# Optimization experiments

Measured on AMD Instinct MI355X. Metric: run time of the kernel, lower is better.

The kernel has to match this reference:

```python
import jax, jax.numpy as jnp
import numpy as np

B, S, H = 4, 2048, 2048          # batch, seq_len, hidden_size
NH, NKV, D = 8, 1, 256           # query heads, kv heads (MQA), head_dim
ROPE_THETA = 10000.0
SCALE = D ** -0.5


def setup_inputs() -> dict:
    key = jax.random.key(0)
    k1, k2, k3 = jax.random.split(key, 3)
    hidden_states = jax.random.normal(k1, (B, S, H), dtype=jnp.float32)
    w_qkv = jax.random.normal(k2, (H, (NH + 2 * NKV) * D), dtype=jnp.float32) * 0.02
    w_o = jax.random.normal(k3, (NH * D, H), dtype=jnp.float32) * 0.02
    positions = jnp.arange(S, dtype=jnp.int32)
    return {"hidden_states": hidden_states, "positions": positions,
            "w_qkv": w_qkv, "w_o": w_o}


def _apply_rope(x, positions):
    # x: [B, S, n_heads, D], neox style: rotate halves
    d2 = D // 2
    inv_freq = 1.0 / (ROPE_THETA ** (jnp.arange(0, d2, dtype=jnp.float32) * 2.0 / D))
    ang = positions.astype(jnp.float32)[:, None] * inv_freq[None, :]      # [S, d2]
    cos = jnp.cos(ang)[None, :, None, :]                                  # [1,S,1,d2]
    sin = jnp.sin(ang)[None, :, None, :]
    x1, x2 = x[..., :d2], x[..., d2:]
    return jnp.concatenate([x1 * cos - x2 * sin, x2 * cos + x1 * sin], axis=-1)


def reference(hidden_states, positions, w_qkv, w_o):
    # fused QKV projection
    qkv = jnp.einsum('bsh,hd->bsd', hidden_states, w_qkv)                 # [B,S,(NH+2NKV)*D]
    q_size, kv_size = NH * D, NKV * D
    q = qkv[..., :q_size].reshape(B, S, NH, D)
    k = qkv[..., q_size:q_size + kv_size].reshape(B, S, NKV, D)
    v = qkv[..., q_size + kv_size:].reshape(B, S, NKV, D)

    q = _apply_rope(q, positions)
    k = _apply_rope(k, positions)

    # expand KV heads for MQA/GQA
    rep = NH // NKV
    k = jnp.repeat(k, rep, axis=2)                                        # [B,S,NH,D]
    v = jnp.repeat(v, rep, axis=2)

    scores = jnp.einsum('bqhd,bkhd->bhqk', q, k) * SCALE                  # [B,NH,S,S]
    causal = jnp.tril(jnp.ones((S, S), dtype=bool))
    scores = jnp.where(causal[None, None], scores, jnp.finfo(scores.dtype).min)
    probs = jax.nn.softmax(scores, axis=-1)
    attn = jnp.einsum('bhqk,bkhd->bqhd', probs, v).reshape(B, S, NH * D)

    return jnp.einsum('bsd,dh->bsh', attn, w_o)                           # [B,S,H]
```

## Files before the change

kernel.cpp:

```cpp
#include <hip/hip_runtime.h>
#include <math.h>

constexpr int BATCH = 4;
constexpr int SEQ   = 2048;
constexpr int HID   = 2048;
constexpr int NHEAD = 8;
constexpr int HD    = 256;
constexpr int QKVN  = (NHEAD + 2) * HD;
constexpr float SCL = 0.0625f;

typedef __bf16 bf16_t;
typedef __bf16 bf16x8 __attribute__((ext_vector_type(8)));
typedef float  f32x4  __attribute__((ext_vector_type(4)));

__device__ __forceinline__ f32x4 zero4() {
  f32x4 z; z[0] = 0.f; z[1] = 0.f; z[2] = 0.f; z[3] = 0.f; return z;
}

__device__ __forceinline__ f32x4 mfma16(bf16x8 a, bf16x8 b, f32x4 c) {
  return __builtin_amdgcn_mfma_f32_16x16x32_bf16(a, b, c, 0, 0, 0);
}

__device__ __forceinline__ void gl2lds16(const void* g, void* lds) {
  typedef __attribute__((address_space(1))) void* gp_t;
  typedef __attribute__((address_space(3))) void* lp_t;
  __builtin_amdgcn_global_load_lds((gp_t)(size_t)g,
                                   (lp_t)(unsigned int)(size_t)lds, 16, 0, 0);
}

__device__ __forceinline__ float rmax16(float v) {
#pragma unroll
  for (int o = 1; o < 16; o <<= 1) v = fmaxf(v, __shfl_xor(v, o));
  return v;
}
__device__ __forceinline__ float rsum16(float v) {
#pragma unroll
  for (int o = 1; o < 16; o <<= 1) v += __shfl_xor(v, o);
  return v;
}

__global__ __launch_bounds__(256)
void cvt_bf16_kernel(const float* __restrict__ in, bf16_t* __restrict__ out) {
  const int i = blockIdx.x * 256 + threadIdx.x;
  const float4 a = ((const float4*)in)[i * 2];
  const float4 b = ((const float4*)in)[i * 2 + 1];
  bf16x8 o;
  o[0] = (bf16_t)a.x; o[1] = (bf16_t)a.y; o[2] = (bf16_t)a.z; o[3] = (bf16_t)a.w;
  o[4] = (bf16_t)b.x; o[5] = (bf16_t)b.y; o[6] = (bf16_t)b.z; o[7] = (bf16_t)b.w;
  ((bf16x8*)out)[i] = o;
}

__global__ __launch_bounds__(256)
void transw_kernel(const float* __restrict__ w, bf16_t* __restrict__ wT, int K, int N) {
  __shared__ __align__(16) bf16_t tile[64][72];
  const int n0 = blockIdx.x * 64, k0 = blockIdx.y * 64;
  const int t = threadIdx.x, rr = t >> 3, c8 = (t & 7) * 8;
#pragma unroll
  for (int it = 0; it < 2; ++it) {
    const int r = rr + it * 32;
    const float4* p = (const float4*)(w + (size_t)(k0 + r) * N + n0 + c8);
    const float4 a = p[0], b = p[1];
    bf16x8 o;
    o[0] = (bf16_t)a.x; o[1] = (bf16_t)a.y; o[2] = (bf16_t)a.z; o[3] = (bf16_t)a.w;
    o[4] = (bf16_t)b.x; o[5] = (bf16_t)b.y; o[6] = (bf16_t)b.z; o[7] = (bf16_t)b.w;
    *(bf16x8*)&tile[r][c8] = o;
  }
  __syncthreads();
#pragma unroll
  for (int it = 0; it < 2; ++it) {
    const int rn = rr + it * 32;
    bf16x8 o;
#pragma unroll
    for (int j = 0; j < 8; ++j) o[j] = tile[c8 + j][rn];
    *(bf16x8*)&wT[(size_t)(n0 + rn) * K + k0 + c8] = o;
  }
}

template <typename TC>
__global__ __launch_bounds__(256)
void gemm_bt_kernel(const bf16_t* __restrict__ A, const bf16_t* __restrict__ BT,
                    TC* __restrict__ C, int M, int N, int K) {
  __shared__ __align__(16) bf16_t As[128 * 32];
  __shared__ __align__(16) bf16_t Bs[128 * 32];
  const int tid = threadIdx.x;
  const int lane = tid & 63, w = tid >> 6;
  const int quad = lane >> 4, l15 = lane & 15;
  const int bm = blockIdx.y * 128, bn = blockIdx.x * 128;
  const int wm = (w & 1) * 64, wn = (w >> 1) * 64;
  const int r0 = tid >> 2, c0 = tid & 3;

  f32x4 acc[4][4];
#pragma unroll
  for (int mt = 0; mt < 4; ++mt)
#pragma unroll
    for (int nt = 0; nt < 4; ++nt) acc[mt][nt] = zero4();

  for (int k0 = 0; k0 < K; k0 += 32) {
#pragma unroll
    for (int i = 0; i < 2; ++i) {
      const int r = r0 + i * 64;
      const int cg = (c0 ^ (r & 3)) << 3;
      gl2lds16(A + (size_t)(bm + r) * K + k0 + cg, &As[(i * 256 + w * 64) * 8]);
      gl2lds16(BT + (size_t)(bn + r) * K + k0 + cg, &Bs[(i * 256 + w * 64) * 8]);
    }
    __syncthreads();
    bf16x8 af[4], bf[4];
#pragma unroll
    for (int mt = 0; mt < 4; ++mt) {
      const int row = wm + mt * 16 + l15;
      af[mt] = *(const bf16x8*)&As[row * 32 + ((quad ^ (row & 3)) << 3)];
    }
#pragma unroll
    for (int nt = 0; nt < 4; ++nt) {
      const int row = wn + nt * 16 + l15;
      bf[nt] = *(const bf16x8*)&Bs[row * 32 + ((quad ^ (row & 3)) << 3)];
    }
#pragma unroll
    for (int mt = 0; mt < 4; ++mt)
#pragma unroll
      for (int nt = 0; nt < 4; ++nt)
        acc[mt][nt] = mfma16(af[mt], bf[nt], acc[mt][nt]);
    __syncthreads();
  }

#pragma unroll
  for (int mt = 0; mt < 4; ++mt)
#pragma unroll
    for (int nt = 0; nt < 4; ++nt)
#pragma unroll
      for (int r = 0; r < 4; ++r) {
        const int row = bm + wm + mt * 16 + quad * 4 + r;
        const int col = bn + wn + nt * 16 + l15;
        C[(size_t)row * N + col] = (TC)acc[mt][nt][r];
      }
}

__global__ __launch_bounds__(128)
void rope_kernel(const int* __restrict__ pos, bf16_t* __restrict__ qkv) {
  const int bs = blockIdx.x, h = blockIdx.y, i = threadIdx.x;
  const int s = bs & (SEQ - 1);
  const float inv_freq = powf(10000.0f, -(float)i / 128.0f);
  const float ang = (float)pos[s] * inv_freq;
  float sn, cs;
  sincosf(ang, &sn, &cs);
  const size_t base = (size_t)bs * QKVN + (size_t)h * HD;
  const float x1 = (float)qkv[base + i];
  const float x2 = (float)qkv[base + 128 + i];
  qkv[base + i]       = (bf16_t)(x1 * cs - x2 * sn);
  qkv[base + 128 + i] = (bf16_t)(x2 * cs + x1 * sn);
}

__global__ __launch_bounds__(256)
void vtrans_kernel(const bf16_t* __restrict__ qkv, bf16_t* __restrict__ Vt) {
  __shared__ __align__(16) bf16_t tile[64][72];
  const int s0 = blockIdx.x * 64, d0 = blockIdx.y * 64, b = blockIdx.z;
  const int t = threadIdx.x, rr = t >> 3, c8 = (t & 7) * 8;
#pragma unroll
  for (int it = 0; it < 2; ++it) {
    const int r = rr + it * 32;
    *(bf16x8*)&tile[r][c8] =
        *(const bf16x8*)&qkv[(size_t)(b * SEQ + s0 + r) * QKVN + 2304 + d0 + c8];
  }
  __syncthreads();
#pragma unroll
  for (int it = 0; it < 2; ++it) {
    const int dd = rr + it * 32;
    bf16x8 o;
#pragma unroll
    for (int j = 0; j < 8; ++j) o[j] = tile[c8 + j][dd];
    *(bf16x8*)&Vt[(size_t)(b * HD + d0 + dd) * SEQ + s0 + c8] = o;
  }
}

__global__ __launch_bounds__(512)
void attn_kernel(const bf16_t* __restrict__ qkv, const bf16_t* __restrict__ Vt,
                 bf16_t* __restrict__ O) {
  __shared__ __align__(16) bf16_t Ks[64 * 256];
  __shared__ __align__(16) bf16_t Vts[256 * 64];
  __shared__ __align__(16) bf16_t Pl[8][16][72];

  const int tid = threadIdx.x, w = tid >> 6, lane = tid & 63;
  const int quad = lane >> 4, l15 = lane & 15;
  const int b = blockIdx.x >> 6;
  const int qtR = blockIdx.x & 63;
  const int h = w;

  const int krow_base = w * 2 + (lane >> 5);
  const int kcol = lane & 31;
  const int vrow_base = w * 8 + (lane >> 3);
  const int vcol = lane & 7;

  for (int phase = 0; phase < 2; ++phase) {
    const int qt = phase ? (127 - qtR) : qtR;
    const int q0 = qt * 16;

    bf16x8 qf[8];
    const bf16_t* qp =
        qkv + (size_t)(b * SEQ + q0 + l15) * QKVN + (size_t)h * HD + quad * 8;
#pragma unroll
    for (int ks = 0; ks < 8; ++ks) qf[ks] = *(const bf16x8*)(qp + ks * 32);

    float mrun[4], lrun[4];
    f32x4 of[16];
#pragma unroll
    for (int r = 0; r < 4; ++r) { mrun[r] = -3e38f; lrun[r] = 0.f; }
#pragma unroll
    for (int dt = 0; dt < 16; ++dt) of[dt] = zero4();

    const int ntiles = q0 / 64 + 1;

    for (int kt = 0; kt < ntiles; ++kt) {
      const bf16_t* kbase = qkv + (size_t)(b * SEQ + kt * 64) * QKVN + 2048;
#pragma unroll
      for (int i = 0; i < 4; ++i) {
        const int r = i * 16 + krow_base;
        gl2lds16(kbase + (size_t)r * QKVN + ((kcol ^ (r & 31)) << 3),
                 &Ks[(i * 512 + w * 64) * 8]);
      }
      const bf16_t* vbase = Vt + (size_t)b * HD * SEQ + kt * 64;
#pragma unroll
      for (int i = 0; i < 4; ++i) {
        const int r = i * 64 + vrow_base;
        gl2lds16(vbase + (size_t)r * SEQ + ((vcol ^ (r & 7)) << 3),
                 &Vts[(i * 512 + w * 64) * 8]);
      }
      __syncthreads();

      f32x4 sf[4];
#pragma unroll
      for (int nt = 0; nt < 4; ++nt) {
        f32x4 acc = zero4();
        const int row = nt * 16 + l15;
#pragma unroll
        for (int ks = 0; ks < 8; ++ks) {
          const int j = ks * 4 + quad;
          const bf16x8 kf = *(const bf16x8*)&Ks[row * 256 + ((j ^ (row & 31)) << 3)];
          acc = mfma16(qf[ks], kf, acc);
        }
        sf[nt] = acc;
      }

      float mx[4];
#pragma unroll
      for (int r = 0; r < 4; ++r) {
        const int qg = q0 + quad * 4 + r;
        float v = -3e38f;
#pragma unroll
        for (int nt = 0; nt < 4; ++nt) {
          const int kg = kt * 64 + nt * 16 + l15;
          const float s = (kg <= qg) ? sf[nt][r] * SCL : -3e38f;
          sf[nt][r] = s;
          v = fmaxf(v, s);
        }
        mx[r] = rmax16(v);
      }
      float al[4];
#pragma unroll
      for (int r = 0; r < 4; ++r) {
        const float mn = fmaxf(mrun[r], mx[r]);
        al[r] = __expf(mrun[r] - mn);
        mrun[r] = mn;
      }
#pragma unroll
      for (int r = 0; r < 4; ++r) {
        float sum = 0.f;
#pragma unroll
        for (int nt = 0; nt < 4; ++nt) {
          const float pv = __expf(sf[nt][r] - mrun[r]);
          Pl[w][quad * 4 + r][nt * 16 + l15] = (bf16_t)pv;
          sum += pv;
        }
        lrun[r] = lrun[r] * al[r] + rsum16(sum);
      }
      __asm__ volatile("s_waitcnt lgkmcnt(0)" ::: "memory");

      f32x4 av;
#pragma unroll
      for (int r = 0; r < 4; ++r) av[r] = al[r];
#pragma unroll
      for (int dt = 0; dt < 16; ++dt) of[dt] *= av;

      bf16x8 pa[2];
#pragma unroll
      for (int k2 = 0; k2 < 2; ++k2)
        pa[k2] = *(const bf16x8*)&Pl[w][l15][k2 * 32 + quad * 8];
#pragma unroll
      for (int dt = 0; dt < 16; ++dt) {
        const int row = dt * 16 + l15;
#pragma unroll
        for (int k2 = 0; k2 < 2; ++k2) {
          const int j = k2 * 4 + quad;
          const bf16x8 vf = *(const bf16x8*)&Vts[row * 64 + ((j ^ (row & 7)) << 3)];
          of[dt] = mfma16(pa[k2], vf, of[dt]);
        }
      }
      __syncthreads();
    }

    f32x4 iv;
#pragma unroll
    for (int r = 0; r < 4; ++r) iv[r] = 1.0f / lrun[r];
#pragma unroll
    for (int dt = 0; dt < 16; ++dt) {
      const f32x4 o = of[dt] * iv;
#pragma unroll
      for (int r = 0; r < 4; ++r)
        O[(size_t)(b * SEQ + q0 + quad * 4 + r) * HID + (size_t)h * HD + dt * 16 + l15] =
            (bf16_t)o[r];
    }
  }
}

extern "C" void kernel_launch(void* const* d_in, const int* in_sizes, int n_in,
                              void* d_out, int out_size, void* d_ws, size_t ws_size,
                              hipStream_t stream) {
  const float* hidden  = (const float*)d_in[0];
  const int* positions = (const int*)d_in[1];
  const float* w_qkv   = (const float*)d_in[2];
  const float* w_o     = (const float*)d_in[3];
  float* out           = (float*)d_out;

  char* ws = (char*)d_ws;
  bf16_t* hiddenB = (bf16_t*)ws; ws += (size_t)8192 * 2048 * 2;
  bf16_t* wqkvT   = (bf16_t*)ws; ws += (size_t)2560 * 2048 * 2;
  bf16_t* woT     = (bf16_t*)ws; ws += (size_t)2048 * 2048 * 2;
  bf16_t* qkvB    = (bf16_t*)ws; ws += (size_t)8192 * 2560 * 2;
  bf16_t* VtB     = (bf16_t*)ws; ws += (size_t)4 * 256 * 2048 * 2;
  bf16_t* attnB   = (bf16_t*)ws;

  cvt_bf16_kernel<<<8192, 256, 0, stream>>>(hidden, hiddenB);
  transw_kernel<<<dim3(QKVN / 64, HID / 64), 256, 0, stream>>>(w_qkv, wqkvT, HID, QKVN);
  transw_kernel<<<dim3(HID / 64, HID / 64), 256, 0, stream>>>(w_o, woT, HID, HID);

  gemm_bt_kernel<bf16_t><<<dim3(QKVN / 128, 64), 256, 0, stream>>>
      (hiddenB, wqkvT, qkvB, 8192, QKVN, HID);

  rope_kernel<<<dim3(BATCH * SEQ, 9), 128, 0, stream>>>(positions, qkvB);
  vtrans_kernel<<<dim3(SEQ / 64, HD / 64, BATCH), 256, 0, stream>>>(qkvB, VtB);

  attn_kernel<<<256, 512, 0, stream>>>(qkvB, VtB, attnB);

  gemm_bt_kernel<float><<<dim3(HID / 128, 64), 256, 0, stream>>>
      (attnB, woT, out, 8192, HID, HID);
}
```

Measured before the change: 545.1 us.

## Double-buffer attention K/V tiles, skip rescale lazily, vectorise RoPE with table

The attention kernel now double-buffers the K and V LDS tiles, so the next tile's global-to-LDS copy is issued before the current tile is computed. Causal masking is applied only on the diagonal tile, and the running-max rescale of the output accumulators is skipped unless some row's max grows by more than 8. RoPE is split into a small cos/sin table kernel plus a vectorised 8-wide apply kernel, which removes per-element sincos and powf. Costs are double the K/V LDS footprint, which may lower occupancy, and a lazy-rescale threshold that lets unscaled exponentials grow up to e^8 before rescaling.

```diff
diff --git a/kernel.cpp b/kernel.cpp
--- a/kernel.cpp
+++ b/kernel.cpp
@@ -136,18 +136,34 @@
 }
 
 __global__ __launch_bounds__(128)
-void rope_kernel(const int* __restrict__ pos, bf16_t* __restrict__ qkv) {
-  const int bs = blockIdx.x, h = blockIdx.y, i = threadIdx.x;
-  const int s = bs & (SEQ - 1);
+void rope_table_kernel(const int* __restrict__ pos, float2* __restrict__ tab) {
+  const int s = blockIdx.x, i = threadIdx.x;
   const float inv_freq = powf(10000.0f, -(float)i / 128.0f);
   const float ang = (float)pos[s] * inv_freq;
   float sn, cs;
   sincosf(ang, &sn, &cs);
+  tab[s * 128 + i] = make_float2(cs, sn);
+}
+
+__global__ __launch_bounds__(256)
+void rope_kernel(const float2* __restrict__ tab, bf16_t* __restrict__ qkv) {
+  const int bs = blockIdx.x * 16 + (threadIdx.x >> 4);
+  const int h  = blockIdx.y;
+  const int i0 = (threadIdx.x & 15) * 8;
+  const int s  = bs & (SEQ - 1);
   const size_t base = (size_t)bs * QKVN + (size_t)h * HD;
-  const float x1 = (float)qkv[base + i];
-  const float x2 = (float)qkv[base + 128 + i];
-  qkv[base + i]       = (bf16_t)(x1 * cs - x2 * sn);
-  qkv[base + 128 + i] = (bf16_t)(x2 * cs + x1 * sn);
+  bf16x8 a = *(const bf16x8*)&qkv[base + i0];
+  bf16x8 b = *(const bf16x8*)&qkv[base + 128 + i0];
+  bf16x8 oa, ob;
+#pragma unroll
+  for (int j = 0; j < 8; ++j) {
+    const float2 t = tab[s * 128 + i0 + j];
+    const float x1 = (float)a[j], x2 = (float)b[j];
+    oa[j] = (bf16_t)(x1 * t.x - x2 * t.y);
+    ob[j] = (bf16_t)(x2 * t.x + x1 * t.y);
+  }
+  *(bf16x8*)&qkv[base + i0]       = oa;
+  *(bf16x8*)&qkv[base + 128 + i0] = ob;
 }
 
 __global__ __launch_bounds__(256)
@@ -175,8 +191,8 @@
 __global__ __launch_bounds__(512)
 void attn_kernel(const bf16_t* __restrict__ qkv, const bf16_t* __restrict__ Vt,
                  bf16_t* __restrict__ O) {
-  __shared__ __align__(16) bf16_t Ks[64 * 256];
-  __shared__ __align__(16) bf16_t Vts[256 * 64];
+  __shared__ __align__(16) bf16_t Ks[2][64 * 256];
+  __shared__ __align__(16) bf16_t Vts[2][256 * 64];
   __shared__ __align__(16) bf16_t Pl[8][16][72];
 
   const int tid = threadIdx.x, w = tid >> 6, lane = tid & 63;
@@ -190,6 +206,26 @@
   const int vrow_base = w * 8 + (lane >> 3);
   const int vcol = lane & 7;
 
+  const bf16_t* kbase0 = qkv + (size_t)(b * SEQ) * QKVN + 2048;
+  const bf16_t* vbase0 = Vt + (size_t)b * HD * SEQ;
+
+  auto stage = [&](int kt, int buf) {
+    const bf16_t* kbase = kbase0 + (size_t)(kt * 64) * QKVN;
+#pragma unroll
+    for (int i = 0; i < 4; ++i) {
+      const int r = i * 16 + krow_base;
+      gl2lds16(kbase + (size_t)r * QKVN + ((kcol ^ (r & 31)) << 3),
+               &Ks[buf][(i * 512 + w * 64) * 8]);
+    }
+    const bf16_t* vbase = vbase0 + kt * 64;
+#pragma unroll
+    for (int i = 0; i < 4; ++i) {
+      const int r = i * 64 + vrow_base;
+      gl2lds16(vbase + (size_t)r * SEQ + ((vcol ^ (r & 7)) << 3),
+               &Vts[buf][(i * 512 + w * 64) * 8]);
+    }
+  };
+
   for (int phase = 0; phase < 2; ++phase) {
     const int qt = phase ? (127 - qtR) : qtR;
     const int q0 = qt * 16;
@@ -208,23 +244,15 @@
     for (int dt = 0; dt < 16; ++dt) of[dt] = zero4();
 
     const int ntiles = q0 / 64 + 1;
+    int cur = 0;
+    stage(0, 0);
+    __syncthreads();
 
     for (int kt = 0; kt < ntiles; ++kt) {
-      const bf16_t* kbase = qkv + (size_t)(b * SEQ + kt * 64) * QKVN + 2048;
-#pragma unroll
-      for (int i = 0; i < 4; ++i) {
-        const int r = i * 16 + krow_base;
-        gl2lds16(kbase + (size_t)r * QKVN + ((kcol ^ (r & 31)) << 3),
-                 &Ks[(i * 512 + w * 64) * 8]);
-      }
-      const bf16_t* vbase = Vt + (size_t)b * HD * SEQ + kt * 64;
-#pragma unroll
-      for (int i = 0; i < 4; ++i) {
-        const int r = i * 64 + vrow_base;
-        gl2lds16(vbase + (size_t)r * SEQ + ((vcol ^ (r & 7)) << 3),
-                 &Vts[(i * 512 + w * 64) * 8]);
-      }
-      __syncthreads();
+      if (kt + 1 < ntiles) stage(kt + 1, cur ^ 1);
+
+      const bf16_t* ksb = Ks[cur];
+      const bf16_t* vsb = Vts[cur];
 
       f32x4 sf[4];
 #pragma unroll
@@ -234,12 +262,13 @@
 #pragma unroll
         for (int ks = 0; ks < 8; ++ks) {
           const int j = ks * 4 + quad;
-          const bf16x8 kf = *(const bf16x8*)&Ks[row * 256 + ((j ^ (row & 31)) << 3)];
+          const bf16x8 kf = *(const bf16x8*)&ksb[row * 256 + ((j ^ (row & 31)) << 3)];
           acc = mfma16(qf[ks], kf, acc);
         }
         sf[nt] = acc;
       }
 
+      const bool lastTile = (kt == ntiles - 1);
       float mx[4];
 #pragma unroll
       for (int r = 0; r < 4; ++r) {
@@ -247,20 +276,32 @@
         float v = -3e38f;
 #pragma unroll
         for (int nt = 0; nt < 4; ++nt) {
-          const int kg = kt * 64 + nt * 16 + l15;
-          const float s = (kg <= qg) ? sf[nt][r] * SCL : -3e38f;
+          float s = sf[nt][r] * SCL;
+          if (lastTile) {
+            const int kg = kt * 64 + nt * 16 + l15;
+            if (kg > qg) s = -3e38f;
+          }
           sf[nt][r] = s;
           v = fmaxf(v, s);
         }
         mx[r] = rmax16(v);
       }
-      float al[4];
-#pragma unroll
-      for (int r = 0; r < 4; ++r) {
-        const float mn = fmaxf(mrun[r], mx[r]);
-        al[r] = __expf(mrun[r] - mn);
-        mrun[r] = mn;
-      }
+
+      float g = 0.f;
+#pragma unroll
+      for (int r = 0; r < 4; ++r) g = fmaxf(g, mx[r] - mrun[r]);
+      const bool resc = !__all(g <= 8.0f);
+      f32x4 av;
+      if (resc) {
+#pragma unroll
+        for (int r = 0; r < 4; ++r) {
+          const float mn = fmaxf(mrun[r], mx[r]);
+          av[r] = __expf(mrun[r] - mn);
+          mrun[r] = mn;
+          lrun[r] *= av[r];
+        }
+      }
+
 #pragma unroll
       for (int r = 0; r < 4; ++r) {
         float sum = 0.f;
@@ -270,15 +311,13 @@
           Pl[w][quad * 4 + r][nt * 16 + l15] = (bf16_t)pv;
           sum += pv;
         }
-        lrun[r] = lrun[r] * al[r] + rsum16(sum);
+        lrun[r] += rsum16(sum);
+      }
+      if (resc) {
+#pragma unroll
+        for (int dt = 0; dt < 16; ++dt) of[dt] *= av;
       }
       __asm__ volatile("s_waitcnt lgkmcnt(0)" ::: "memory");
-
-      f32x4 av;
-#pragma unroll
-      for (int r = 0; r < 4; ++r) av[r] = al[r];
-#pragma unroll
-      for (int dt = 0; dt < 16; ++dt) of[dt] *= av;
 
       bf16x8 pa[2];
 #pragma unroll
@@ -290,11 +329,13 @@
 #pragma unroll
         for (int k2 = 0; k2 < 2; ++k2) {
           const int j = k2 * 4 + quad;
-          const bf16x8 vf = *(const bf16x8*)&Vts[row * 64 + ((j ^ (row & 7)) << 3)];
+          const bf16x8 vf = *(const bf16x8*)&vsb[row * 64 + ((j ^ (row & 7)) << 3)];
           of[dt] = mfma16(pa[k2], vf, of[dt]);
         }
       }
+
       __syncthreads();
+      cur ^= 1;
     }
 
     f32x4 iv;
@@ -328,14 +369,17 @@
   bf16_t* VtB     = (bf16_t*)ws; ws += (size_t)4 * 256 * 2048 * 2;
   bf16_t* attnB   = (bf16_t*)ws;
 
+  float2* ropeTab = (float2*)attnB;
+
   cvt_bf16_kernel<<<8192, 256, 0, stream>>>(hidden, hiddenB);
   transw_kernel<<<dim3(QKVN / 64, HID / 64), 256, 0, stream>>>(w_qkv, wqkvT, HID, QKVN);
   transw_kernel<<<dim3(HID / 64, HID / 64), 256, 0, stream>>>(w_o, woT, HID, HID);
+  rope_table_kernel<<<SEQ, 128, 0, stream>>>(positions, ropeTab);
 
   gemm_bt_kernel<bf16_t><<<dim3(QKVN / 128, 64), 256, 0, stream>>>
       (hiddenB, wqkvT, qkvB, 8192, QKVN, HID);
 
-  rope_kernel<<<dim3(BATCH * SEQ, 9), 128, 0, stream>>>(positions, qkvB);
+  rope_kernel<<<dim3(BATCH * SEQ / 16, 9), 256, 0, stream>>>(ropeTab, qkvB);
   vtrans_kernel<<<dim3(SEQ / 64, HD / 64, BATCH), 256, 0, stream>>>(qkvB, VtB);
 
   attn_kernel<<<256, 512, 0, stream>>>(qkvB, VtB, attnB);
```

New measurement: 510.0 us. 6.5% less time.
